# Kernel tuning notes

Measured on AMD Instinct MI355X. Metric: run time of the kernel, lower is better.

## Reference

```python
import jax, jax.numpy as jnp
import numpy as np

B, N, C, H = 8, 1024, 512, 8
EPS = 1e-6


def setup_inputs() -> dict:
    key = jax.random.key(0)
    k0, k1, k2, k3, k4 = jax.random.split(key, 5)
    x = jax.random.normal(k0, (B, N, C), dtype=jnp.float32)
    # nonnegative random-walk visit-frequency mask stand-in
    mask = jax.random.uniform(k1, (N, N), dtype=jnp.float32)
    w_qkv = jax.random.normal(k2, (C, 3 * C), dtype=jnp.float32) * 0.02
    w_out = jax.random.normal(k3, (C, C), dtype=jnp.float32) * 0.02
    b_out = jax.random.normal(k4, (C,), dtype=jnp.float32) * 0.02
    return {"x": x, "mask": mask, "w_qkv": w_qkv, "w_out": w_out, "b_out": b_out}


def reference(x, mask, w_qkv, w_out, b_out):
    b, n, c = x.shape
    d = c // H
    qkv = x @ w_qkv                                   # [B,N,3C]
    q, k, v = jnp.split(qkv, 3, axis=-1)

    def to_heads(t):
        return t.reshape(b, n, H, d).transpose(0, 2, 1, 3)  # [B,H,N,D]

    q, k, v = to_heads(q), to_heads(k), to_heads(v)
    # positive feature map
    q = jax.nn.relu(q) + EPS
    k = jax.nn.relu(k) + EPS
    # graph diffusion: (q^T @ mask)^T == einsum over source node m
    q = q + 0.1 * jnp.einsum('bhmd,mn->bhnd', q, mask)
    k = k + 0.1 * jnp.einsum('bhmd,mn->bhnd', k, mask)
    # linear kernel scores, elementwise-masked
    kernel = jnp.einsum('bhnd,bhmd->bhnm', q, k) * mask   # [B,H,N,N]
    z = 1.0 / (kernel.sum(axis=-1, keepdims=True) + EPS)  # [B,H,N,1]
    out = jnp.einsum('bhnm,bhmd->bhnd', kernel, v) * z    # [B,H,N,D]
    out = out.transpose(0, 2, 1, 3).reshape(b, n, c)      # [B,N,C]
    return out @ w_out + b_out
```

## Files before the change

kernel.cpp:

```cpp
#include <hip/hip_runtime.h>
#include <cstddef>

#define Bsz 8
#define Nn  1024
#define Cc  512
#define Hh  8
#define Dd  64
#define EPSF 1e-6f

typedef __attribute__((ext_vector_type(8))) short short8;
typedef __attribute__((ext_vector_type(4))) float floatx4;

static __device__ __forceinline__ short f2bf(float f) {
    union { float f; unsigned u; } v; v.f = f;
    unsigned r = (v.u + 0x7FFFu + ((v.u >> 16) & 1u)) >> 16;
    return (short)r;
}
static __device__ __forceinline__ float bf2f(short s) {
    union { unsigned u; float f; } v; v.u = ((unsigned)(unsigned short)s) << 16;
    return v.f;
}

#define GLOAD_LDS16(gp, lp)                                              \
    __builtin_amdgcn_global_load_lds(                                    \
        (const __attribute__((address_space(1))) void*)(gp),             \
        (__attribute__((address_space(3))) void*)(lp), 16, 0, 0)

static __device__ __forceinline__
void stage_tile(short* __restrict__ lds, const short* __restrict__ src,
                int ldsrc, int tid, int CHUNKS, int SLOTS) {
    #pragma unroll
    for (int s = tid; s < SLOTS; s += 256) {
        int r = s / CHUNKS, cs = s % CHUNKS;
        int gc = cs ^ (r & 7);
        GLOAD_LDS16(&src[(size_t)r * ldsrc + gc * 8], &lds[s * 8]);
    }
}
static __device__ __forceinline__
short8 fragT(const short* __restrict__ lds, int CHUNKS, int r, int lc) {
    return *(const short8*)&lds[(r * CHUNKS + (lc ^ (r & 7))) * 8];
}

#define FENCE() asm volatile("" ::: "memory")
#define BARRIER_RAW() do { FENCE(); __builtin_amdgcn_s_barrier(); FENCE(); } while (0)
#define WAITVM(N) asm volatile("s_waitcnt vmcnt(" #N ")" ::: "memory")
#define WAITLGKM0() asm volatile("s_waitcnt lgkmcnt(0)" ::: "memory")

__global__ __launch_bounds__(256)
void prep_all(const float* __restrict__ x, const float* __restrict__ mask,
              const float* __restrict__ wq, const float* __restrict__ wo,
              short* __restrict__ xb, short* __restrict__ Ad,
              short* __restrict__ wqT, short* __restrict__ woT,
              short* __restrict__ mbf) {
    __shared__ float t[64][65];
    const int tid = threadIdx.x;
    const int bid = blockIdx.x;

    if (bid < 2048) {
        int idx = bid * 256 + tid;
        const float* s = &x[(size_t)idx * 8];
        union { short h[8]; int4 v; } u;
        #pragma unroll
        for (int j = 0; j < 8; j++) u.h[j] = f2bf(s[j]);
        *(int4*)&xb[(size_t)idx * 8] = u.v;
        return;
    }
    if (bid < 2304) {
        int idx = bid - 2048;
        const int n0 = (idx & 15) * 64, m0 = (idx >> 4) * 64;
        #pragma unroll
        for (int i = 0; i < 4; i++) {
            int k = i * 256 + tid;
            int r = k >> 4, c4 = (k & 15) * 4;
            *(float4*)&t[r][c4] = *(const float4*)&mask[(size_t)(m0 + r) * Nn + n0 + c4];
        }
        __syncthreads();
        #pragma unroll
        for (int i = 0; i < 4; i++) {
            int k = i * 256 + tid;
            int rr = k >> 4, c4 = (k & 15) * 4;
            union { short h[4]; int2 v; } u;
            #pragma unroll
            for (int j = 0; j < 4; j++) {
                int mm = c4 + j;
                float v = 0.1f * t[mm][rr] + ((n0 + rr) == (m0 + mm) ? 1.0f : 0.0f);
                u.h[j] = f2bf(v);
            }
            *(int2*)&Ad[(size_t)(n0 + rr) * Nn + m0 + c4] = u.v;
        }
        return;
    }
    if (bid < 2496) {
        int idx = bid - 2304;
        const int n0 = (idx % 24) * 64, k0 = (idx / 24) * 64;
        #pragma unroll
        for (int i = 0; i < 4; i++) {
            int k = i * 256 + tid;
            int r = k >> 4, c4 = (k & 15) * 4;
            *(float4*)&t[r][c4] = *(const float4*)&wq[(size_t)(k0 + r) * 1536 + n0 + c4];
        }
        __syncthreads();
        #pragma unroll
        for (int i = 0; i < 4; i++) {
            int k = i * 256 + tid;
            int rr = k >> 4, c4 = (k & 15) * 4;
            union { short h[4]; int2 v; } u;
            #pragma unroll
            for (int j = 0; j < 4; j++) u.h[j] = f2bf(t[c4 + j][rr]);
            *(int2*)&wqT[(size_t)(n0 + rr) * 512 + k0 + c4] = u.v;
        }
        return;
    }
    if (bid < 2560) {
        int idx = bid - 2496;
        const int n0 = (idx & 7) * 64, k0 = (idx >> 3) * 64;
        #pragma unroll
        for (int i = 0; i < 4; i++) {
            int k = i * 256 + tid;
            int r = k >> 4, c4 = (k & 15) * 4;
            *(float4*)&t[r][c4] = *(const float4*)&wo[(size_t)(k0 + r) * 512 + n0 + c4];
        }
        __syncthreads();
        #pragma unroll
        for (int i = 0; i < 4; i++) {
            int k = i * 256 + tid;
            int rr = k >> 4, c4 = (k & 15) * 4;
            union { short h[4]; int2 v; } u;
            #pragma unroll
            for (int j = 0; j < 4; j++) u.h[j] = f2bf(t[c4 + j][rr]);
            *(int2*)&woT[(size_t)(n0 + rr) * 512 + k0 + c4] = u.v;
        }
        return;
    }
    {
        int idx = (bid - 2560) * 256 + tid;
        const float* s = &mask[(size_t)idx * 8];
        union { short h[8]; int4 v; } u;
        #pragma unroll
        for (int j = 0; j < 8; j++) u.h[j] = f2bf(s[j]);
        *(int4*)&mbf[(size_t)idx * 8] = u.v;
    }
}

static __device__ __forceinline__
void stageA_half(short* __restrict__ buf, const short* __restrict__ gA,
                 int kt, int h, int tid) {
    #pragma unroll
    for (int kk = 0; kk < 2; kk++) {
        int i = tid + kk * 512;
        int run = i >> 9;
        int within = i & 511;
        int r = run * 128 + h * 64 + (within >> 3);
        int c = within & 7;
        int gc = c ^ (r & 7);
        GLOAD_LDS16(gA + (size_t)r * 512 + kt + gc * 8, buf + (r * 8 + c) * 8);
    }
}
static __device__ __forceinline__
void stageB_half(short* __restrict__ buf, const short* __restrict__ gB,
                 int kt, int h, int tid) {
    #pragma unroll
    for (int kk = 0; kk < 2; kk++) {
        int i = tid + kk * 512;
        int run = i >> 8;
        int within = i & 255;
        int r = run * 64 + h * 32 + (within >> 3);
        int c = within & 7;
        int gc = c ^ (r & 7);
        GLOAD_LDS16(gB + (size_t)r * 512 + kt + gc * 8, buf + (r * 8 + c) * 8);
    }
}

template<int MH>
static __device__ __forceinline__
void readA8(const short* __restrict__ bufA, short8 (&aF)[4][2],
            int wr, int l16, int quad) {
    #pragma unroll
    for (int f = 0; f < 4; f++)
        #pragma unroll
        for (int kk = 0; kk < 2; kk++)
            aF[f][kk] = fragT(bufA, 8, wr * 128 + MH * 64 + f * 16 + l16, kk * 4 + quad);
}
template<int NH>
static __device__ __forceinline__
void readB4(const short* __restrict__ bufB, short8 (&bF)[2][2],
            int wc, int l16, int quad) {
    #pragma unroll
    for (int g = 0; g < 2; g++)
        #pragma unroll
        for (int kk = 0; kk < 2; kk++)
            bF[g][kk] = fragT(bufB, 8, wc * 64 + NH * 32 + g * 16 + l16, kk * 4 + quad);
}
template<int MH, int NH>
static __device__ __forceinline__
void mfma16(short8 (&aF)[4][2], short8 (&bF)[2][2], floatx4 (&acc)[8][4]) {
    #pragma unroll
    for (int kk = 0; kk < 2; kk++)
        #pragma unroll
        for (int f = 0; f < 4; f++)
            #pragma unroll
            for (int g = 0; g < 2; g++)
                acc[MH * 4 + f][NH * 2 + g] = __builtin_amdgcn_mfma_f32_16x16x32_bf16(
                    aF[f][kk], bF[g][kk], acc[MH * 4 + f][NH * 2 + g], 0, 0, 0);
}

__global__ __launch_bounds__(512, 2)
void gemm_qkv(const short* __restrict__ xb, const short* __restrict__ wqT,
              short* __restrict__ qT, short* __restrict__ kT,
              short* __restrict__ vT) {
    extern __shared__ short smem[];

    const int tid = threadIdx.x;
    const int lin = blockIdx.x;
    const int wgid = (lin & 7) * 24 + (lin >> 3);
    const int mt = wgid / 6, nt = wgid % 6;
    const int m0 = mt * 256, n0 = nt * 256;

    const int wid = tid >> 6, lane = tid & 63;
    const int quad = lane >> 4, l16 = lane & 15;
    const int wr = wid >> 2, wc = wid & 3;

    const short* Ab = xb  + (size_t)m0 * 512;
    const short* Bb = wqT + (size_t)n0 * 512;

    floatx4 acc[8][4];
    #pragma unroll
    for (int i = 0; i < 8; i++)
        #pragma unroll
        for (int j = 0; j < 4; j++) acc[i][j] = (floatx4){0.f, 0.f, 0.f, 0.f};

    short8 aF[4][2], bF[2][2];

    stageA_half(smem,          Ab, 0, 0, tid);
    stageB_half(smem + 16384,  Bb, 0, 0, tid);
    stageA_half(smem,          Ab, 0, 1, tid);
    stageB_half(smem + 16384,  Bb, 0, 1, tid);
    WAITVM(4); BARRIER_RAW();

    for (int j = 0; j < 8; ++j) {
        const short* cA = smem + (j & 1) * 32768;
        const short* cB = cA + 16384;
        short* nA = smem + ((j + 1) & 1) * 32768;
        short* nB = nA + 16384;
        const int kn = ((j + 1) & 7) * 64;

        readA8<0>(cA, aF, wr, l16, quad);
        readB4<0>(cB, bF, wc, l16, quad);
        stageA_half(nA, Ab, kn, 0, tid);
        stageB_half(nB, Bb, kn, 0, tid);
        BARRIER_RAW();
        __builtin_amdgcn_s_setprio(1);
        mfma16<0, 0>(aF, bF, acc);
        __builtin_amdgcn_s_setprio(0);
        WAITVM(4); BARRIER_RAW();

        readA8<1>(cA, aF, wr, l16, quad);
        stageA_half(nA, Ab, kn, 1, tid);
        stageB_half(nB, Bb, kn, 1, tid);
        BARRIER_RAW();
        __builtin_amdgcn_s_setprio(1);
        mfma16<1, 0>(aF, bF, acc);
        __builtin_amdgcn_s_setprio(0);
        BARRIER_RAW();

        readB4<1>(cB, bF, wc, l16, quad);
        BARRIER_RAW();
        __builtin_amdgcn_s_setprio(1);
        mfma16<1, 1>(aF, bF, acc);
        __builtin_amdgcn_s_setprio(0);
        BARRIER_RAW();

        readA8<0>(cA, aF, wr, l16, quad);
        BARRIER_RAW();
        __builtin_amdgcn_s_setprio(1);
        mfma16<0, 1>(aF, bF, acc);
        __builtin_amdgcn_s_setprio(0);
        WAITVM(4); BARRIER_RAW();
    }

    WAITVM(0); BARRIER_RAW();

    short* T = smem + wid * 8192;
    const int doRelu = (n0 < 1024);
    #pragma unroll
    for (int mf = 0; mf < 8; mf++)
        #pragma unroll
        for (int nf = 0; nf < 4; nf++)
            #pragma unroll
            for (int rr = 0; rr < 4; rr++) {
                float v = acc[mf][nf][rr];
                if (doRelu) v = fmaxf(v, 0.0f) + EPSF;
                int row = nf * 16 + l16;
                int col = mf * 16 + quad * 4 + rr;
                T[row * 128 + (col ^ ((row & 15) << 3))] = f2bf(v);
            }
    const int gm0 = m0 + wr * 128;
    const int b = gm0 >> 10, m_in0 = gm0 & 1023;
    #pragma unroll
    for (int g = 0; g < 4; g++) {
        int row = (lane >> 2) + g * 16;
        int gn = n0 + wc * 64 + row;
        int part = gn >> 9, ci = gn & 511;
        short* base = (part == 0) ? qT : (part == 1) ? kT : vT;
        short* dst = base + ((size_t)b * 512 + ci) * 1024 + m_in0;
        #pragma unroll
        for (int cc = 0; cc < 4; cc++) {
            int cs = ((lane & 3) + cc * 4) * 8;
            *(int4*)&dst[cs] = *(const int4*)&T[row * 128 + (cs ^ ((row & 15) << 3))];
        }
    }
}

static __device__ __forceinline__
void dstageA_half(short* __restrict__ buf, const short* __restrict__ gA,
                  int kt, int h, int tid) {
    #pragma unroll
    for (int kk = 0; kk < 2; kk++) {
        int i = tid + kk * 512;
        int rl = i >> 3;
        int c  = i & 7;
        int r  = (rl >> 5) * 64 + h * 32 + (rl & 31);
        int gc = c ^ (r & 7);
        GLOAD_LDS16(gA + (size_t)r * 1024 + kt + gc * 8, buf + (r * 8 + c) * 8);
    }
}
static __device__ __forceinline__
void dstageB_half(short* __restrict__ buf, const short* __restrict__ gB,
                  int kt, int h, int tid) {
    int rl = tid >> 3;
    int c  = tid & 7;
    int r  = (rl >> 5) * 64 + h * 32 + (rl & 31);
    int gc = c ^ (r & 7);
    GLOAD_LDS16(gB + (size_t)r * 1024 + kt + gc * 8, buf + (r * 8 + c) * 8);
}
template<int MH>
static __device__ __forceinline__
void dreadA(const short* __restrict__ bufA, short8 (&aF)[2][2],
            int wr, int l16, int quad) {
    #pragma unroll
    for (int f = 0; f < 2; f++)
        #pragma unroll
        for (int kk = 0; kk < 2; kk++)
            aF[f][kk] = fragT(bufA, 8, wr * 64 + MH * 32 + f * 16 + l16, kk * 4 + quad);
}
template<int NH>
static __device__ __forceinline__
void dreadB(const short* __restrict__ bufB, short8 (&bF)[2][2],
            int wc, int l16, int quad) {
    #pragma unroll
    for (int g = 0; g < 2; g++)
        #pragma unroll
        for (int kk = 0; kk < 2; kk++)
            bF[g][kk] = fragT(bufB, 8, wc * 64 + NH * 32 + g * 16 + l16, kk * 4 + quad);
}
template<int MH, int NH>
static __device__ __forceinline__
void dmfma8(short8 (&aF)[2][2], short8 (&bF)[2][2], floatx4 (&acc)[4][4]) {
    #pragma unroll
    for (int kk = 0; kk < 2; kk++)
        #pragma unroll
        for (int f = 0; f < 2; f++)
            #pragma unroll
            for (int g = 0; g < 2; g++)
                acc[MH * 2 + f][NH * 2 + g] = __builtin_amdgcn_mfma_f32_16x16x32_bf16(
                    aF[f][kk], bF[g][kk], acc[MH * 2 + f][NH * 2 + g], 0, 0, 0);
}

__global__ __launch_bounds__(512, 2)
void gemm_diff8(const short* __restrict__ Ad, const short* __restrict__ qT,
                const short* __restrict__ kT, short* __restrict__ qd,
                short* __restrict__ kd) {
    extern __shared__ short smem[];

    const int tid = threadIdx.x;
    const int lin = blockIdx.x;
    const int wgid = (lin & 7) * 32 + (lin >> 3);
    const int mt = wgid >> 6, ct = wgid & 63;
    const int m0 = mt * 256;
    const int seg = ct >> 2, cb = (ct & 3) * 128;
    const int b = seg >> 1, part = seg & 1;

    const short* Bb = ((part ? kT : qT) + (size_t)b * 512 * 1024) + (size_t)cb * 1024;
    short* outb = (part ? kd : qd) + (size_t)b * 1024 * 512;
    const short* Abase = Ad + (size_t)m0 * 1024;

    const int wid = tid >> 6, lane = tid & 63;
    const int quad = lane >> 4, l16 = lane & 15;
    const int wr = wid >> 1, wc = wid & 1;

    floatx4 acc[4][4];
    #pragma unroll
    for (int i = 0; i < 4; i++)
        #pragma unroll
        for (int j = 0; j < 4; j++) acc[i][j] = (floatx4){0.f, 0.f, 0.f, 0.f};

    short8 aF[2][2], bF[2][2];

    dstageA_half(smem,          Abase, 0, 0, tid);
    dstageB_half(smem + 16384,  Bb,    0, 0, tid);
    dstageA_half(smem,          Abase, 0, 1, tid);
    dstageB_half(smem + 16384,  Bb,    0, 1, tid);
    WAITVM(3); BARRIER_RAW();

    for (int j = 0; j < 16; ++j) {
        const short* cA = smem + (j & 1) * 24576;
        const short* cB = cA + 16384;
        short* nA = smem + ((j + 1) & 1) * 24576;
        short* nB = nA + 16384;
        const int kn = ((j + 1) & 15) * 64;

        dreadA<0>(cA, aF, wr, l16, quad);
        dreadB<0>(cB, bF, wc, l16, quad);
        dstageA_half(nA, Abase, kn, 0, tid);
        dstageB_half(nB, Bb,    kn, 0, tid);
        BARRIER_RAW();
        __builtin_amdgcn_s_setprio(1);
        dmfma8<0, 0>(aF, bF, acc);
        __builtin_amdgcn_s_setprio(0);
        WAITVM(3); BARRIER_RAW();

        dreadA<1>(cA, aF, wr, l16, quad);
        dstageA_half(nA, Abase, kn, 1, tid);
        dstageB_half(nB, Bb,    kn, 1, tid);
        BARRIER_RAW();
        __builtin_amdgcn_s_setprio(1);
        dmfma8<1, 0>(aF, bF, acc);
        __builtin_amdgcn_s_setprio(0);
        BARRIER_RAW();

        dreadB<1>(cB, bF, wc, l16, quad);
        BARRIER_RAW();
        __builtin_amdgcn_s_setprio(1);
        dmfma8<1, 1>(aF, bF, acc);
        __builtin_amdgcn_s_setprio(0);
        BARRIER_RAW();

        dreadA<0>(cA, aF, wr, l16, quad);
        BARRIER_RAW();
        __builtin_amdgcn_s_setprio(1);
        dmfma8<0, 1>(aF, bF, acc);
        __builtin_amdgcn_s_setprio(0);
        WAITVM(3); BARRIER_RAW();
    }
    WAITVM(0);

    #pragma unroll
    for (int fr = 0; fr < 4; fr++)
        #pragma unroll
        for (int rr = 0; rr < 4; rr++) {
            int n = m0 + wr * 64 + fr * 16 + quad * 4 + rr;
            #pragma unroll
            for (int fc = 0; fc < 4; fc++) {
                int c = cb + wc * 64 + fc * 16 + l16;
                outb[(size_t)n * 512 + c] = f2bf(acc[fr][fc][rr]);
            }
        }
}

static __device__ __forceinline__
void attn_qk(const short* __restrict__ ks, short* __restrict__ pb,
             const int2 (&M)[2][4], const short8 (&aT)[2][2],
             float (&dreg)[2], int wave, int quad, int l16) {
    const int ssrow[2] = { wave * 32 + l16, wave * 32 + 16 + l16 };
    #pragma unroll
    for (int mt = 0; mt < 4; mt++) {
        const short8 k0f = fragT(ks, 8, mt * 16 + l16, quad);
        const short8 k1f = fragT(ks, 8, mt * 16 + l16, 4 + quad);
        #pragma unroll
        for (int t = 0; t < 2; t++) {
            floatx4 s = (floatx4){0.f, 0.f, 0.f, 0.f};
            s = __builtin_amdgcn_mfma_f32_16x16x32_bf16(k0f, aT[t][0], s, 0, 0, 0);
            s = __builtin_amdgcn_mfma_f32_16x16x32_bf16(k1f, aT[t][1], s, 0, 0, 0);
            const int row = ssrow[t];
            const int c = mt * 16 + quad * 4;
            const int off = (row * 8 + ((c >> 3) ^ (row & 7))) * 8 + (c & 7);
            union { short hh[4]; int2 v; } mk; mk.v = M[t][mt];
            float sv0 = s[0] * bf2f(mk.hh[0]);
            float sv1 = s[1] * bf2f(mk.hh[1]);
            float sv2 = s[2] * bf2f(mk.hh[2]);
            float sv3 = s[3] * bf2f(mk.hh[3]);
            dreg[t] += (sv0 + sv1) + (sv2 + sv3);
            int lo, hi;
            asm("v_cvt_pk_bf16_f32 %0, %1, %2" : "=v"(lo) : "v"(sv0), "v"(sv1));
            asm("v_cvt_pk_bf16_f32 %0, %1, %2" : "=v"(hi) : "v"(sv2), "v"(sv3));
            int2 pv; pv.x = lo; pv.y = hi;
            *(int2*)&pb[off] = pv;
        }
    }
}
static __device__ __forceinline__
void attn_pv(const short* __restrict__ vt, const short* __restrict__ pb,
             floatx4 (&nacc)[2][4], int wave, int quad, int l16) {
    short8 p[2][2];
    #pragma unroll
    for (int t = 0; t < 2; t++) {
        p[t][0] = fragT(pb, 8, wave * 32 + t * 16 + l16, quad);
        p[t][1] = fragT(pb, 8, wave * 32 + t * 16 + l16, 4 + quad);
    }
    __builtin_amdgcn_s_setprio(1);
    #pragma unroll
    for (int dt = 0; dt < 4; dt++) {
        const short8 v0 = fragT(vt, 8, dt * 16 + l16, quad);
        const short8 v1 = fragT(vt, 8, dt * 16 + l16, 4 + quad);
        #pragma unroll
        for (int t = 0; t < 2; t++) {
            nacc[t][dt] = __builtin_amdgcn_mfma_f32_16x16x32_bf16(p[t][0], v0, nacc[t][dt], 0, 0, 0);
            nacc[t][dt] = __builtin_amdgcn_mfma_f32_16x16x32_bf16(p[t][1], v1, nacc[t][dt], 0, 0, 0);
        }
    }
    __builtin_amdgcn_s_setprio(0);
}

__global__ __launch_bounds__(256)
void attn_mfma(const short* __restrict__ qd, const short* __restrict__ kd,
               const short* __restrict__ vTg, const short* __restrict__ mbf,
               short* __restrict__ abf) {
    extern __shared__ short smem[];
    short* qss = smem;
    short* ps  = smem + 8192;
    short* kv0 = smem + 16384;
    short* kv1 = smem + 24576;

    const int tid = threadIdx.x;
    const int bh = blockIdx.x;
    const int b = bh >> 3, h = bh & 7;
    const int n0 = blockIdx.y * 128;

    const int wave = tid >> 6, lane = tid & 63;
    const int quad = lane >> 4, l16 = lane & 15;

    const short* Qb = qd + ((size_t)b * Nn + n0) * Cc + h * Dd;
    const short* Kb = kd + (size_t)b * Nn * Cc + h * Dd;
    const short* Vb = vTg + ((size_t)b * Cc + h * Dd) * Nn;
    const short* baseM = mbf + (size_t)(n0 + wave * 32 + l16) * Nn + quad * 4;

    stage_tile(qss, Qb, Cc, tid, 8, 1024);
    stage_tile(kv0,        Kb, Cc, tid, 8, 512);
    stage_tile(kv0 + 4096, Vb, Nn, tid, 8, 512);
    int2 Ma[2][4], Mb2[2][4];
    #pragma unroll
    for (int t = 0; t < 2; t++)
        #pragma unroll
        for (int mt = 0; mt < 4; mt++)
            Ma[t][mt] = *(const int2*)(baseM + t * 16 * Nn + mt * 16);
    WAITVM(0); BARRIER_RAW();

    short8 aT[2][2];
    #pragma unroll
    for (int t = 0; t < 2; t++) {
        aT[t][0] = fragT(qss, 8, wave * 32 + t * 16 + l16, quad);
        aT[t][1] = fragT(qss, 8, wave * 32 + t * 16 + l16, 4 + quad);
    }

    float dreg[2] = {0.f, 0.f};
    floatx4 nacc[2][4];
    #pragma unroll
    for (int t = 0; t < 2; t++)
        #pragma unroll
        for (int i = 0; i < 4; i++) nacc[t][i] = (floatx4){0.f, 0.f, 0.f, 0.f};

    for (int jo = 0; jo < 8; jo++) {
        const int j0 = 2 * jo;
        {
            stage_tile(kv1,        Kb + (size_t)(j0 + 1) * 64 * Cc, Cc, tid, 8, 512);
            stage_tile(kv1 + 4096, Vb + (j0 + 1) * 64,              Nn, tid, 8, 512);
            #pragma unroll
            for (int t = 0; t < 2; t++)
                #pragma unroll
                for (int mt = 0; mt < 4; mt++)
                    Mb2[t][mt] = *(const int2*)(baseM + t * 16 * Nn + (j0 + 1) * 64 + mt * 16);
            WAITVM(12);
        }
        attn_qk(kv0, ps, Ma, aT, dreg, wave, quad, l16);
        attn_pv(kv0 + 4096, ps, nacc, wave, quad, l16);
        BARRIER_RAW();

        if (jo < 7) {
            stage_tile(kv0,        Kb + (size_t)(j0 + 2) * 64 * Cc, Cc, tid, 8, 512);
            stage_tile(kv0 + 4096, Vb + (j0 + 2) * 64,              Nn, tid, 8, 512);
            #pragma unroll
            for (int t = 0; t < 2; t++)
                #pragma unroll
                for (int mt = 0; mt < 4; mt++)
                    Ma[t][mt] = *(const int2*)(baseM + t * 16 * Nn + (j0 + 2) * 64 + mt * 16);
            WAITVM(12);
        } else {
            WAITVM(0);
        }
        attn_qk(kv1, ps, Mb2, aT, dreg, wave, quad, l16);
        attn_pv(kv1 + 4096, ps, nacc, wave, quad, l16);
        BARRIER_RAW();
    }

    #pragma unroll
    for (int t = 0; t < 2; t++) {
        dreg[t] += __shfl_xor(dreg[t], 16, 64);
        dreg[t] += __shfl_xor(dreg[t], 32, 64);
    }

    #pragma unroll
    for (int t = 0; t < 2; t++)
        #pragma unroll
        for (int r = 0; r < 4; r++) {
            int nloc = quad * 4 + r;
            float den = __shfl(dreg[t], nloc, 64);
            int n = n0 + wave * 32 + t * 16 + nloc;
            float zr = 1.0f / (den + EPSF);
            #pragma unroll
            for (int dt = 0; dt < 4; dt++) {
                size_t o = ((size_t)b * Nn + n) * Cc + h * Dd + dt * 16 + l16;
                abf[o] = f2bf(nacc[t][dt][r] * zr);
            }
        }
}

__global__ __launch_bounds__(256)
void gemm_out(const short* __restrict__ abf, const short* __restrict__ woT,
              const float* __restrict__ bias, float* __restrict__ out) {
    __shared__ short smem[12288];
    short* As = smem;
    short* Bs = smem + 4096;

    const int tid = threadIdx.x;
    const int m0 = blockIdx.y * 64;
    const int n0 = blockIdx.x * 128;
    const int wave = tid >> 6, lane = tid & 63;
    const int quad = lane >> 4, l16 = lane & 15;
    const int wm = (wave >> 1) * 32, wn = (wave & 1) * 64;

    floatx4 acc[2][4];
    #pragma unroll
    for (int i = 0; i < 2; i++)
        #pragma unroll
        for (int j = 0; j < 4; j++) acc[i][j] = (floatx4){0.f, 0.f, 0.f, 0.f};

    const short* Ab = abf + (size_t)m0 * 512;
    const short* Bb = woT + (size_t)n0 * 512;

    for (int k0 = 0; k0 < 512; k0 += 64) {
        __syncthreads();
        stage_tile(As, Ab + k0, 512, tid, 8, 512);
        stage_tile(Bs, Bb + k0, 512, tid, 8, 1024);
        __syncthreads();
        #pragma unroll
        for (int kh = 0; kh < 2; kh++) {
            short8 a[2], b[4];
            #pragma unroll
            for (int i = 0; i < 2; i++)
                a[i] = fragT(As, 8, wm + i * 16 + l16, kh * 4 + quad);
            #pragma unroll
            for (int i = 0; i < 4; i++)
                b[i] = fragT(Bs, 8, wn + i * 16 + l16, kh * 4 + quad);
            #pragma unroll
            for (int mi = 0; mi < 2; mi++)
                #pragma unroll
                for (int ni = 0; ni < 4; ni++)
                    acc[mi][ni] = __builtin_amdgcn_mfma_f32_16x16x32_bf16(
                        a[mi], b[ni], acc[mi][ni], 0, 0, 0);
        }
    }

    #pragma unroll
    for (int mi = 0; mi < 2; mi++)
        #pragma unroll
        for (int r = 0; r < 4; r++) {
            int m = m0 + wm + mi * 16 + quad * 4 + r;
            #pragma unroll
            for (int ni = 0; ni < 4; ni++) {
                int n = n0 + wn + ni * 16 + l16;
                out[(size_t)m * 512 + n] = acc[mi][ni][r] + bias[n];
            }
        }
}

extern "C" void kernel_launch(void* const* d_in, const int* in_sizes, int n_in,
                              void* d_out, int out_size, void* d_ws, size_t ws_size,
                              hipStream_t stream) {
    const float* x     = (const float*)d_in[0];
    const float* mask  = (const float*)d_in[1];
    const float* w_qkv = (const float*)d_in[2];
    const float* w_out = (const float*)d_in[3];
    const float* b_out = (const float*)d_in[4];
    float* out = (float*)d_out;

    char* p = (char*)d_ws;
    short* xb  = (short*)p; p += 8388608;
    short* wqT = (short*)p; p += 1572864;
    short* Ad  = (short*)p; p += 2097152;
    short* woT = (short*)p; p += 524288;
    short* mbf = (short*)p; p += 2097152;
    short* qT  = (short*)p; p += 8388608;
    short* kT  = (short*)p; p += 8388608;
    short* vT  = (short*)p; p += 8388608;
    short* qd  = (short*)p; p += 8388608;
    short* kd  = (short*)p; p += 8388608;
    short* abf = (short*)p; p += 8388608;

    static int attr_set = 0;
    if (!attr_set) {
        hipFuncSetAttribute(reinterpret_cast<const void*>(gemm_qkv),
                            hipFuncAttributeMaxDynamicSharedMemorySize, 131072);
        hipFuncSetAttribute(reinterpret_cast<const void*>(gemm_diff8),
                            hipFuncAttributeMaxDynamicSharedMemorySize, 98304);
        hipFuncSetAttribute(reinterpret_cast<const void*>(attn_mfma),
                            hipFuncAttributeMaxDynamicSharedMemorySize, 65536);
        attr_set = 1;
    }

    dim3 blk(256);

    prep_all  <<<3072, blk, 0, stream>>>(x, mask, w_qkv, w_out,
                                         xb, Ad, wqT, woT, mbf);
    gemm_qkv  <<<dim3(192), dim3(512), 131072, stream>>>(xb, wqT, qT, kT, vT);
    gemm_diff8<<<dim3(256), dim3(512), 98304, stream>>>(Ad, qT, kT, qd, kd);
    attn_mfma <<<dim3(64, 8), dim3(256), 65536, stream>>>(qd, kd, vT, mbf, abf);
    gemm_out  <<<dim3(4, 128), blk, 0, stream>>>(abf, woT, b_out, out);
}
```

Before: 176.5 us.

## Load attention K/V/Q fragments directly into registers instead of LDS staging

The attention kernel stops staging Q, K and V tiles through shared memory with global_load_lds and block barriers. Each wave now loads its own MFMA fragments straight from global memory into registers, double-buffering K and the mask across iterations. LDS is kept only as a per-wave P buffer, so block barriers disappear and LDS use drops enough to allow higher occupancy (launch bounds of 2 blocks per SM). The trade-off is that all four waves of a block fetch the same K/V fragments redundantly through the cache, and register pressure rises.

```diff
diff --git a/kernel.cpp b/kernel.cpp
--- a/kernel.cpp
+++ b/kernel.cpp
@@ -44,7 +44,6 @@
 #define FENCE() asm volatile("" ::: "memory")
 #define BARRIER_RAW() do { FENCE(); __builtin_amdgcn_s_barrier(); FENCE(); } while (0)
 #define WAITVM(N) asm volatile("s_waitcnt vmcnt(" #N ")" ::: "memory")
-#define WAITLGKM0() asm volatile("s_waitcnt lgkmcnt(0)" ::: "memory")
 
 __global__ __launch_bounds__(256)
 void prep_all(const float* __restrict__ x, const float* __restrict__ mask,
@@ -458,19 +457,45 @@
 }
 
 static __device__ __forceinline__
-void attn_qk(const short* __restrict__ ks, short* __restrict__ pb,
-             const int2 (&M)[2][4], const short8 (&aT)[2][2],
-             float (&dreg)[2], int wave, int quad, int l16) {
+void aload_k(short8 (&K)[4][2], const short* __restrict__ Kb, int j,
+             int quad, int l16) {
+    #pragma unroll
+    for (int mt = 0; mt < 4; mt++)
+        #pragma unroll
+        for (int kk = 0; kk < 2; kk++)
+            K[mt][kk] = *(const short8*)(Kb +
+                (size_t)(j * 64 + mt * 16 + l16) * Cc + (kk * 4 + quad) * 8);
+}
+static __device__ __forceinline__
+void aload_m(int2 (&M)[2][4], const short* __restrict__ baseM, int j) {
+    #pragma unroll
+    for (int t = 0; t < 2; t++)
+        #pragma unroll
+        for (int mt = 0; mt < 4; mt++)
+            M[t][mt] = *(const int2*)(baseM + (size_t)t * 16 * Nn + j * 64 + mt * 16);
+}
+static __device__ __forceinline__
+void aload_v(short8 (&V)[4][2], const short* __restrict__ Vb, int j,
+             int quad, int l16) {
+    #pragma unroll
+    for (int dt = 0; dt < 4; dt++)
+        #pragma unroll
+        for (int kk = 0; kk < 2; kk++)
+            V[dt][kk] = *(const short8*)(Vb +
+                (size_t)(dt * 16 + l16) * Nn + j * 64 + (kk * 4 + quad) * 8);
+}
+static __device__ __forceinline__
+void attn_qk_r(const short8 (&K)[4][2], const int2 (&M)[2][4],
+               const short8 (&aT)[2][2], short* __restrict__ pb,
+               float (&dreg)[2], int wave, int quad, int l16) {
     const int ssrow[2] = { wave * 32 + l16, wave * 32 + 16 + l16 };
     #pragma unroll
     for (int mt = 0; mt < 4; mt++) {
-        const short8 k0f = fragT(ks, 8, mt * 16 + l16, quad);
-        const short8 k1f = fragT(ks, 8, mt * 16 + l16, 4 + quad);
         #pragma unroll
         for (int t = 0; t < 2; t++) {
             floatx4 s = (floatx4){0.f, 0.f, 0.f, 0.f};
-            s = __builtin_amdgcn_mfma_f32_16x16x32_bf16(k0f, aT[t][0], s, 0, 0, 0);
-            s = __builtin_amdgcn_mfma_f32_16x16x32_bf16(k1f, aT[t][1], s, 0, 0, 0);
+            s = __builtin_amdgcn_mfma_f32_16x16x32_bf16(K[mt][0], aT[t][0], s, 0, 0, 0);
+            s = __builtin_amdgcn_mfma_f32_16x16x32_bf16(K[mt][1], aT[t][1], s, 0, 0, 0);
             const int row = ssrow[t];
             const int c = mt * 16 + quad * 4;
             const int off = (row * 8 + ((c >> 3) ^ (row & 7))) * 8 + (c & 7);
@@ -489,8 +514,8 @@
     }
 }
 static __device__ __forceinline__
-void attn_pv(const short* __restrict__ vt, const short* __restrict__ pb,
-             floatx4 (&nacc)[2][4], int wave, int quad, int l16) {
+void attn_pv_r(const short8 (&V)[4][2], const short* __restrict__ pb,
+               floatx4 (&nacc)[2][4], int wave, int quad, int l16) {
     short8 p[2][2];
     #pragma unroll
     for (int t = 0; t < 2; t++) {
@@ -500,26 +525,20 @@
     __builtin_amdgcn_s_setprio(1);
     #pragma unroll
     for (int dt = 0; dt < 4; dt++) {
-        const short8 v0 = fragT(vt, 8, dt * 16 + l16, quad);
-        const short8 v1 = fragT(vt, 8, dt * 16 + l16, 4 + quad);
         #pragma unroll
         for (int t = 0; t < 2; t++) {
-            nacc[t][dt] = __builtin_amdgcn_mfma_f32_16x16x32_bf16(p[t][0], v0, nacc[t][dt], 0, 0, 0);
-            nacc[t][dt] = __builtin_amdgcn_mfma_f32_16x16x32_bf16(p[t][1], v1, nacc[t][dt], 0, 0, 0);
+            nacc[t][dt] = __builtin_amdgcn_mfma_f32_16x16x32_bf16(p[t][0], V[dt][0], nacc[t][dt], 0, 0, 0);
+            nacc[t][dt] = __builtin_amdgcn_mfma_f32_16x16x32_bf16(p[t][1], V[dt][1], nacc[t][dt], 0, 0, 0);
         }
     }
     __builtin_amdgcn_s_setprio(0);
 }
 
-__global__ __launch_bounds__(256)
+__global__ __launch_bounds__(256, 2)
 void attn_mfma(const short* __restrict__ qd, const short* __restrict__ kd,
                const short* __restrict__ vTg, const short* __restrict__ mbf,
                short* __restrict__ abf) {
-    extern __shared__ short smem[];
-    short* qss = smem;
-    short* ps  = smem + 8192;
-    short* kv0 = smem + 16384;
-    short* kv1 = smem + 24576;
+    __shared__ short ps[8192];
 
     const int tid = threadIdx.x;
     const int bh = blockIdx.x;
@@ -534,23 +553,18 @@
     const short* Vb = vTg + ((size_t)b * Cc + h * Dd) * Nn;
     const short* baseM = mbf + (size_t)(n0 + wave * 32 + l16) * Nn + quad * 4;
 
-    stage_tile(qss, Qb, Cc, tid, 8, 1024);
-    stage_tile(kv0,        Kb, Cc, tid, 8, 512);
-    stage_tile(kv0 + 4096, Vb, Nn, tid, 8, 512);
-    int2 Ma[2][4], Mb2[2][4];
+    short8 aT[2][2];
     #pragma unroll
     for (int t = 0; t < 2; t++)
         #pragma unroll
-        for (int mt = 0; mt < 4; mt++)
-            Ma[t][mt] = *(const int2*)(baseM + t * 16 * Nn + mt * 16);
-    WAITVM(0); BARRIER_RAW();
-
-    short8 aT[2][2];
-    #pragma unroll
-    for (int t = 0; t < 2; t++) {
-        aT[t][0] = fragT(qss, 8, wave * 32 + t * 16 + l16, quad);
-        aT[t][1] = fragT(qss, 8, wave * 32 + t * 16 + l16, 4 + quad);
-    }
+        for (int kk = 0; kk < 2; kk++)
+            aT[t][kk] = *(const short8*)(Qb +
+                (size_t)(wave * 32 + t * 16 + l16) * Cc + (kk * 4 + quad) * 8);
+
+    short8 KA[4][2], KB[4][2];
+    int2 MA[2][4], MB[2][4];
+    aload_k(KA, Kb, 0, quad, l16);
+    aload_m(MA, baseM, 0);
 
     float dreg[2] = {0.f, 0.f};
     floatx4 nacc[2][4];
@@ -562,34 +576,21 @@
     for (int jo = 0; jo < 8; jo++) {
         const int j0 = 2 * jo;
         {
-            stage_tile(kv1,        Kb + (size_t)(j0 + 1) * 64 * Cc, Cc, tid, 8, 512);
-            stage_tile(kv1 + 4096, Vb + (j0 + 1) * 64,              Nn, tid, 8, 512);
-            #pragma unroll
-            for (int t = 0; t < 2; t++)
-                #pragma unroll
-                for (int mt = 0; mt < 4; mt++)
-                    Mb2[t][mt] = *(const int2*)(baseM + t * 16 * Nn + (j0 + 1) * 64 + mt * 16);
-            WAITVM(12);
-        }
-        attn_qk(kv0, ps, Ma, aT, dreg, wave, quad, l16);
-        attn_pv(kv0 + 4096, ps, nacc, wave, quad, l16);
-        BARRIER_RAW();
-
-        if (jo < 7) {
-            stage_tile(kv0,        Kb + (size_t)(j0 + 2) * 64 * Cc, Cc, tid, 8, 512);
-            stage_tile(kv0 + 4096, Vb + (j0 + 2) * 64,              Nn, tid, 8, 512);
-            #pragma unroll
-            for (int t = 0; t < 2; t++)
-                #pragma unroll
-                for (int mt = 0; mt < 4; mt++)
-                    Ma[t][mt] = *(const int2*)(baseM + t * 16 * Nn + (j0 + 2) * 64 + mt * 16);
-            WAITVM(12);
-        } else {
-            WAITVM(0);
-        }
-        attn_qk(kv1, ps, Mb2, aT, dreg, wave, quad, l16);
-        attn_pv(kv1 + 4096, ps, nacc, wave, quad, l16);
-        BARRIER_RAW();
+            short8 Vr[4][2];
+            aload_v(Vr, Vb, j0, quad, l16);
+            aload_k(KB, Kb, j0 + 1, quad, l16);
+            aload_m(MB, baseM, j0 + 1);
+            attn_qk_r(KA, MA, aT, ps, dreg, wave, quad, l16);
+            attn_pv_r(Vr, ps, nacc, wave, quad, l16);
+        }
+        {
+            short8 Vr[4][2];
+            aload_v(Vr, Vb, j0 + 1, quad, l16);
+            aload_k(KA, Kb, (j0 + 2) & 15, quad, l16);
+            aload_m(MA, baseM, (j0 + 2) & 15);
+            attn_qk_r(KB, MB, aT, ps, dreg, wave, quad, l16);
+            attn_pv_r(Vr, ps, nacc, wave, quad, l16);
+        }
     }
 
     #pragma unroll
@@ -702,8 +703,6 @@
                             hipFuncAttributeMaxDynamicSharedMemorySize, 131072);
         hipFuncSetAttribute(reinterpret_cast<const void*>(gemm_diff8),
                             hipFuncAttributeMaxDynamicSharedMemorySize, 98304);
-        hipFuncSetAttribute(reinterpret_cast<const void*>(attn_mfma),
-                            hipFuncAttributeMaxDynamicSharedMemorySize, 65536);
         attr_set = 1;
     }
 
@@ -713,6 +712,6 @@
                                          xb, Ad, wqT, woT, mbf);
     gemm_qkv  <<<dim3(192), dim3(512), 131072, stream>>>(xb, wqT, qT, kT, vT);
     gemm_diff8<<<dim3(256), dim3(512), 98304, stream>>>(Ad, qT, kT, qd, kd);
-    attn_mfma <<<dim3(64, 8), dim3(256), 65536, stream>>>(qd, kd, vT, mbf, abf);
+    attn_mfma <<<dim3(64, 8), dim3(256), 0, stream>>>(qd, kd, vT, mbf, abf);
     gemm_out  <<<dim3(4, 128), blk, 0, stream>>>(abf, woT, b_out, out);
 }
```

Measured after the change: 224.7 us. 1.27x slower.
